# Kernel optimization log

Hardware: AMD Instinct MI355X
Metric: run time of the kernel (lower is better)

Reference implementation:

```python
import jax, jax.numpy as jnp
import numpy as np

B, S, IN, H, L = 512, 1024, 64, 32, 4


def setup_inputs() -> dict:
    key = jax.random.key(0)
    ks = jax.random.split(key, 9)
    s = 1.0 / np.sqrt(H)  # PyTorch RNN/Linear init scale
    u = lambda k, shape: jax.random.uniform(k, shape, jnp.float32, -s, s)
    return {
        "x": jax.random.normal(ks[0], (B, S, IN), jnp.float32),
        "h_state": jnp.zeros((L, B, H), jnp.float32),
        "W_ih0": u(ks[1], (H, IN)),          # layer 0 input weights
        "W_ih_rest": u(ks[2], (L - 1, H, H)),  # layers 1..3 input weights
        "W_hh": u(ks[3], (L, H, H)),
        "b_ih": u(ks[4], (L, H)),
        "b_hh": u(ks[5], (L, H)),
        "fc_w": u(ks[6], (1, H)),
        "fc_b": u(ks[7], (1,)),
    }


def _rnn_layer(seq_sbf, h0, W_ih, W_hh, b):
    # seq_sbf: [S, B, F]; vanilla RNN: h_t = tanh(x_t W_ih^T + h_{t-1} W_hh^T + b)
    def step(h, x_t):
        h = jnp.tanh(x_t @ W_ih.T + h @ W_hh.T + b)
        return h, h
    return jax.lax.scan(step, h0, seq_sbf)


def reference(x, h_state, W_ih0, W_ih_rest, W_hh, b_ih, b_hh, fc_w, fc_b):
    seq = jnp.swapaxes(x, 0, 1)  # [S, B, IN]
    h_finals = []
    for l in range(L):  # fixed small layer count
        W_ih = W_ih0 if l == 0 else W_ih_rest[l - 1]
        h_last, seq = _rnn_layer(seq, h_state[l], W_ih, W_hh[l], b_ih[l] + b_hh[l])
        h_finals.append(h_last)
    r_out = jnp.swapaxes(seq, 0, 1)                 # [B, S, H]
    logits = (r_out @ fc_w.T + fc_b)[..., 0]        # fused per-timestep Linear -> [B, S]
    probs = jax.nn.softmax(logits, axis=-1)         # nn.Softmax over last (seq) dim
    return probs, jnp.stack(h_finals, axis=0)       # [B,S], [L,B,H]
```

## Files before the change

kernel.cpp:

```cpp
#include <hip/hip_runtime.h>


#define BB 512
#define SS 1024
#define INF 64
#define HH 32
#define LL 4

typedef __fp16 v2h __attribute__((ext_vector_type(2)));

__device__ __forceinline__ v2h bch(unsigned u) { return __builtin_bit_cast(v2h, u); }
__device__ __forceinline__ unsigned bcu(v2h h) { return __builtin_bit_cast(unsigned, h); }

template <int CTRL>
__device__ __forceinline__ float dpp_add(float v) {
  int y = __builtin_amdgcn_update_dpp(0, __float_as_int(v), CTRL, 0xF, 0xF, true);
  return v + __int_as_float(y);
}
template <int CTRL>
__device__ __forceinline__ float dpp_mov(float v) {
  int y = __builtin_amdgcn_update_dpp(0, __float_as_int(v), CTRL, 0xF, 0xF, true);
  return __int_as_float(y);
}

__device__ __forceinline__ float tanh_fast(float a) {
  const float e = __builtin_amdgcn_exp2f(a * 2.885390081777927f);
  const float r = __builtin_amdgcn_rcpf(e + 1.0f);
  return __builtin_fmaf(-2.0f, r, 1.0f);
}

__device__ __forceinline__ float dot16p(const v2h* w, const v2h* v) {
  float a = 0.f, c = 0.f;
#pragma unroll
  for (int j = 0; j < 4; ++j) {
    a = __builtin_amdgcn_fdot2(w[2 * j + 0], v[2 * j + 0], a, false);
    c = __builtin_amdgcn_fdot2(w[2 * j + 1], v[2 * j + 1], c, false);
  }
  return a + c;
}

#define BAR() asm volatile("s_waitcnt lgkmcnt(0)\n\ts_barrier" ::: "memory")

__global__ __launch_bounds__(256) void u0_kernel(
    const float* __restrict__ x, const float* __restrict__ W_ih0,
    const float* __restrict__ b_ih, const float* __restrict__ b_hh,
    float* __restrict__ u0) {
  __shared__ float Wl[HH * INF];
  __shared__ float bl[HH];
  const int tid = threadIdx.x;
  {
    const float4* src = (const float4*)W_ih0;
    float4* dst = (float4*)Wl;
    dst[tid] = src[tid];
    dst[tid + 256] = src[tid + 256];
    if (tid < HH) bl[tid] = b_ih[tid] + b_hh[tid];
  }
  __syncthreads();

  const int row = blockIdx.x * 256 + tid;
  const float4* xr = (const float4*)(x + (size_t)row * INF);
  float acc[HH];
#pragma unroll
  for (int u = 0; u < HH; ++u) acc[u] = bl[u];
#pragma unroll 4
  for (int kc = 0; kc < 16; ++kc) {
    const float4 xv = xr[kc];
#pragma unroll
    for (int u = 0; u < HH; ++u) {
      const float4 wv = ((const float4*)Wl)[u * 16 + kc];
      acc[u] += wv.x * xv.x + wv.y * xv.y + wv.z * xv.z + wv.w * xv.w;
    }
  }
  float4* op = (float4*)(u0 + (size_t)row * HH);
#pragma unroll
  for (int j = 0; j < 8; ++j)
    op[j] = make_float4(acc[4 * j], acc[4 * j + 1], acc[4 * j + 2], acc[4 * j + 3]);
}

__global__ __launch_bounds__(256, 2) void rnn_kernel(
    const float* __restrict__ u0g_all, const float* __restrict__ h_state,
    const float* __restrict__ W_ih_rest, const float* __restrict__ W_hh,
    const float* __restrict__ b_ih, const float* __restrict__ b_hh,
    const float* __restrict__ fc_w, const float* __restrict__ fc_b,
    float* __restrict__ out) {
  __shared__ int hb[LL][2][8][16];
  __shared__ float h3f[2][8][32];
  __shared__ float lbuf[64];

  const int tid  = threadIdx.x;
  const int wid  = tid >> 6;
  const int lane = tid & 63;
  const int b    = blockIdx.x;
  const int ks   = lane & 1;
  const int h    = lane >> 1;

  v2h wih[8], whh[8];
  {
    const float2* ph = (const float2*)(W_hh + (size_t)(wid * HH + h) * HH + ks * 16);
#pragma unroll
    for (int j = 0; j < 8; ++j) whh[j] = __builtin_amdgcn_cvt_pkrtz(ph[j].x, ph[j].y);
  }
  float bias = 0.f;
  if (wid > 0) {
    const float2* pi =
        (const float2*)(W_ih_rest + (size_t)((wid - 1) * HH + h) * HH + ks * 16);
#pragma unroll
    for (int j = 0; j < 8; ++j) wih[j] = __builtin_amdgcn_cvt_pkrtz(pi[j].x, pi[j].y);
    bias = b_ih[wid * HH + h] + b_hh[wid * HH + h];
  }
  const float fcwh = fc_w[h] * 0.5f;
  const float fcb  = fc_b[0];

  v2h sv[8];
  {
    const float2* hs = (const float2*)(h_state + (size_t)(wid * BB + b) * HH);
#pragma unroll
    for (int j = 0; j < 8; ++j)
      sv[j] = __builtin_amdgcn_cvt_pkrtz(hs[ks * 8 + j].x, hs[ks * 8 + j].y);
  }

  const float* ug = u0g_all + (size_t)b * SS * HH;
  float* const outrow = out + (size_t)b * SS;
  float* const hfin   = out + (size_t)BB * SS;

  auto ld8 = [&](const int* p, v2h* v) __attribute__((always_inline)) {
    const uint4* q = (const uint4*)p;
    uint4 A = q[0], B = q[1];
    v[0] = bch(A.x); v[1] = bch(A.y); v[2] = bch(A.z); v[3] = bch(A.w);
    v[4] = bch(B.x); v[5] = bch(B.y); v[6] = bch(B.z); v[7] = bch(B.w);
  };
  auto packpair = [&](float hv) __attribute__((always_inline)) {
    return bcu(__builtin_amdgcn_cvt_pkrtz(hv, dpp_mov<0xEE>(hv)));
  };
  auto store_pk = [&](int l, int buf, int slot, unsigned pk) __attribute__((always_inline)) {
    if ((lane & 3) == 0) hb[l][buf][slot][lane >> 2] = (int)pk;
  };
  auto fcred = [&](float v) __attribute__((always_inline)) {
    v = dpp_add<0x111>(v);
    v = dpp_add<0x112>(v);
    v = dpp_add<0x114>(v);
    v = dpp_add<0x118>(v);
    v = dpp_add<0x142>(v);
    v = dpp_add<0x143>(v);
    return v;
  };

  if (wid == 0) {
    float urA[8], urB[8];
#pragma unroll
    for (int i = 0; i < 8; ++i) urA[i] = ug[i * HH + h];
    auto iter0 = [&](int n, int buf, float* urC, float* urN)
        __attribute__((always_inline)) {
      BAR();
      const bool fc_on = (n >= 4);
      const bool cw    = (n <= 127);
      float a[8];
      if (fc_on) {
#pragma unroll
        for (int i = 0; i < 8; ++i) a[i] = h3f[buf ^ 1][i][h];
      }
      if (cw) {
        const int tb = 8 * (n + 1);
#pragma unroll
        for (int i = 0; i < 8; ++i) {
          int t = tb + i; t = t < SS ? t : SS - 1;
          urN[i] = ug[t * HH + h];
        }
        float hv7 = 0.f;
#pragma unroll
        for (int i = 0; i < 8; ++i) {
          float acc = dot16p(whh, sv);
          acc = dpp_add<0xB1>(acc) + urC[i];
          const float hv = tanh_fast(acc);
          const unsigned pk = packpair(hv);
          store_pk(0, buf, i, pk);
          ld8(&hb[0][buf][i][ks * 8], sv);
          if (i == 7) hv7 = hv;
        }
        if (n == 127 && ks == 0) hfin[(0 * BB + b) * HH + h] = hv7;
      }
      if (fc_on) {
        const int tf0 = 8 * (n - 4);
#pragma unroll
        for (int i = 0; i < 8; ++i) {
          float v = fcred(a[i] * fcwh);
          if (lane == 63) lbuf[(tf0 + i) & 63] = v + fcb;
        }
        if (((n - 4) & 7) == 7) {
          float lv = lbuf[lane];
          outrow[(tf0 + 7) - 63 + lane] = lv;
        }
      }
    };
    for (int n0 = 0; n0 < 132; n0 += 2) {
      iter0(n0, 0, urA, urB);
      iter0(n0 + 1, 1, urB, urA);
    }
  } else {
    v2h vi[8][8];
    auto iterl = [&](int n, int buf) __attribute__((always_inline)) {
      BAR();
      const bool cw = (n >= wid && n <= 127 + wid);
      if (cw) {
#pragma unroll
        for (int i = 0; i < 8; ++i)
          ld8(&hb[wid - 1][buf ^ 1][i][ks * 8], vi[i]);
        float hv7 = 0.f;
#pragma unroll
        for (int i = 0; i < 8; ++i) {
          float acc = dot16p(wih, vi[i]) + dot16p(whh, sv);
          acc = dpp_add<0xB1>(acc) + bias;
          const float hv = tanh_fast(acc);
          const unsigned pk = packpair(hv);
          store_pk(wid, buf, i, pk);
          if (wid == 3 && ks == 0) h3f[buf][i][h] = hv;
          ld8(&hb[wid][buf][i][ks * 8], sv);
          if (i == 7) hv7 = hv;
        }
        if (n == 127 + wid && ks == 0) hfin[(wid * BB + b) * HH + h] = hv7;
      }
    };
    for (int n0 = 0; n0 < 132; n0 += 2) {
      iterl(n0, 0);
      iterl(n0 + 1, 1);
    }
  }
}

__global__ __launch_bounds__(256) void softmax_kernel(float* __restrict__ out) {
  __shared__ float red[8];
  const int row = blockIdx.x;
  float* p = out + (size_t)row * SS;
  const int tid = threadIdx.x;
  float4 v = ((const float4*)p)[tid];
  float m = fmaxf(fmaxf(v.x, v.y), fmaxf(v.z, v.w));
#pragma unroll
  for (int d = 32; d >= 1; d >>= 1) m = fmaxf(m, __shfl_xor(m, d));
  if ((tid & 63) == 0) red[tid >> 6] = m;
  __syncthreads();
  m = fmaxf(fmaxf(red[0], red[1]), fmaxf(red[2], red[3]));
  const float e0 = __expf(v.x - m), e1 = __expf(v.y - m);
  const float e2 = __expf(v.z - m), e3 = __expf(v.w - m);
  float s = (e0 + e1) + (e2 + e3);
#pragma unroll
  for (int d = 32; d >= 1; d >>= 1) s += __shfl_xor(s, d);
  if ((tid & 63) == 0) red[4 + (tid >> 6)] = s;
  __syncthreads();
  s = (red[4] + red[5]) + (red[6] + red[7]);
  const float inv = 1.0f / s;
  float4 o;
  o.x = e0 * inv; o.y = e1 * inv; o.z = e2 * inv; o.w = e3 * inv;
  ((float4*)p)[tid] = o;
}

extern "C" void kernel_launch(void* const* d_in, const int* in_sizes, int n_in,
                              void* d_out, int out_size, void* d_ws, size_t ws_size,
                              hipStream_t stream) {
  const float* x         = (const float*)d_in[0];
  const float* h_state   = (const float*)d_in[1];
  const float* W_ih0     = (const float*)d_in[2];
  const float* W_ih_rest = (const float*)d_in[3];
  const float* W_hh      = (const float*)d_in[4];
  const float* b_ih      = (const float*)d_in[5];
  const float* b_hh      = (const float*)d_in[6];
  const float* fc_w      = (const float*)d_in[7];
  const float* fc_b      = (const float*)d_in[8];
  float* out = (float*)d_out;
  float* u0  = (float*)d_ws;

  hipLaunchKernelGGL(u0_kernel, dim3((BB * SS) / 256), dim3(256), 0, stream,
                     x, W_ih0, b_ih, b_hh, u0);
  hipLaunchKernelGGL(rnn_kernel, dim3(BB), dim3(256), 0, stream,
                     u0, h_state, W_ih_rest, W_hh, b_ih, b_hh, fc_w, fc_b, out);
  hipLaunchKernelGGL(softmax_kernel, dim3(BB), dim3(256), 0, stream, out);
}
```

Baseline: 439.5 us.

## Double wavefront chunk size and fuse softmax into RNN kernel via shared logits

Raises the per-barrier timestep chunk from 8 to 16, which halves the number of block barriers in the layer-pipelined recurrence. Logits are now kept in a full shared-memory row instead of being flushed to global memory, and the softmax runs at the end of the RNN kernel, so the separate softmax launch and its global round trip go away. Layers 1-3 load the previous layer's inputs in groups of four with double buffering to limit register pressure. The trade-offs are a longer pipeline fill/drain per chunk, higher register and LDS use that may hurt occupancy, and more serial work after each barrier.

```diff
diff --git a/kernel.cpp b/kernel.cpp
--- a/kernel.cpp
+++ b/kernel.cpp
@@ -6,6 +6,7 @@
 #define INF 64
 #define HH 32
 #define LL 4
+#define KB 16
 
 typedef __fp16 v2h __attribute__((ext_vector_type(2)));
 
@@ -83,9 +84,10 @@
     const float* __restrict__ b_ih, const float* __restrict__ b_hh,
     const float* __restrict__ fc_w, const float* __restrict__ fc_b,
     float* __restrict__ out) {
-  __shared__ int hb[LL][2][8][16];
-  __shared__ float h3f[2][8][32];
-  __shared__ float lbuf[64];
+  __shared__ int hb[LL][2][KB][16];
+  __shared__ float h3f[2][KB][32];
+  __shared__ float lrow[SS];
+  __shared__ float red[8];
 
   const int tid  = threadIdx.x;
   const int wid  = tid >> 6;
@@ -120,8 +122,7 @@
   }
 
   const float* ug = u0g_all + (size_t)b * SS * HH;
-  float* const outrow = out + (size_t)b * SS;
-  float* const hfin   = out + (size_t)BB * SS;
+  float* const hfin = out + (size_t)BB * SS;
 
   auto ld8 = [&](const int* p, v2h* v) __attribute__((always_inline)) {
     const uint4* q = (const uint4*)p;
@@ -146,111 +147,119 @@
   };
 
   if (wid == 0) {
-    float urA[8], urB[8];
-#pragma unroll
-    for (int i = 0; i < 8; ++i) urA[i] = ug[i * HH + h];
+    float urA[KB], urB[KB];
+#pragma unroll
+    for (int i = 0; i < KB; ++i) urA[i] = ug[i * HH + h];
     auto iter0 = [&](int n, int buf, float* urC, float* urN)
         __attribute__((always_inline)) {
       BAR();
       const bool fc_on = (n >= 4);
-      const bool cw    = (n <= 127);
-      float a[8];
+      const bool cw    = (n <= 63);
+      float a[KB];
       if (fc_on) {
 #pragma unroll
-        for (int i = 0; i < 8; ++i) a[i] = h3f[buf ^ 1][i][h];
+        for (int i = 0; i < KB; ++i) a[i] = h3f[buf ^ 1][i][h];
       }
       if (cw) {
-        const int tb = 8 * (n + 1);
-#pragma unroll
-        for (int i = 0; i < 8; ++i) {
+        const int tb = KB * (n + 1);
+#pragma unroll
+        for (int i = 0; i < KB; ++i) {
           int t = tb + i; t = t < SS ? t : SS - 1;
           urN[i] = ug[t * HH + h];
         }
-        float hv7 = 0.f;
-#pragma unroll
-        for (int i = 0; i < 8; ++i) {
+        float hvL = 0.f;
+#pragma unroll
+        for (int i = 0; i < KB; ++i) {
           float acc = dot16p(whh, sv);
           acc = dpp_add<0xB1>(acc) + urC[i];
           const float hv = tanh_fast(acc);
           const unsigned pk = packpair(hv);
           store_pk(0, buf, i, pk);
           ld8(&hb[0][buf][i][ks * 8], sv);
-          if (i == 7) hv7 = hv;
+          if (i == KB - 1) hvL = hv;
         }
-        if (n == 127 && ks == 0) hfin[(0 * BB + b) * HH + h] = hv7;
+        if (n == 63 && ks == 0) hfin[(0 * BB + b) * HH + h] = hvL;
       }
       if (fc_on) {
-        const int tf0 = 8 * (n - 4);
-#pragma unroll
-        for (int i = 0; i < 8; ++i) {
+        const int tf0 = KB * (n - 4);
+#pragma unroll
+        for (int i = 0; i < KB; ++i) {
           float v = fcred(a[i] * fcwh);
-          if (lane == 63) lbuf[(tf0 + i) & 63] = v + fcb;
+          if (lane == 63) lrow[tf0 + i] = v + fcb;
         }
-        if (((n - 4) & 7) == 7) {
-          float lv = lbuf[lane];
-          outrow[(tf0 + 7) - 63 + lane] = lv;
-        }
-      }
-    };
-    for (int n0 = 0; n0 < 132; n0 += 2) {
+      }
+    };
+    for (int n0 = 0; n0 < 68; n0 += 2) {
       iter0(n0, 0, urA, urB);
       iter0(n0 + 1, 1, urB, urA);
     }
   } else {
-    v2h vi[8][8];
+    v2h viA[4][8], viB[4][8];
+    auto ldgrp = [&](int buf, int g, v2h (*vv)[8]) __attribute__((always_inline)) {
+#pragma unroll
+      for (int q = 0; q < 4; ++q)
+        ld8(&hb[wid - 1][buf ^ 1][g * 4 + q][ks * 8], vv[q]);
+    };
+    auto dogrp = [&](int n, int buf, int g, v2h (*vc)[8], float& hvL)
+        __attribute__((always_inline)) {
+#pragma unroll
+      for (int q = 0; q < 4; ++q) {
+        const int i = g * 4 + q;
+        float accA = dot16p(wih, vc[q]);
+        float acc = accA + dot16p(whh, sv);
+        acc = dpp_add<0xB1>(acc) + bias;
+        const float hv = tanh_fast(acc);
+        const unsigned pk = packpair(hv);
+        store_pk(wid, buf, i, pk);
+        if (wid == 3 && ks == 0) h3f[buf][i][h] = hv;
+        ld8(&hb[wid][buf][i][ks * 8], sv);
+        if (i == KB - 1) hvL = hv;
+      }
+    };
     auto iterl = [&](int n, int buf) __attribute__((always_inline)) {
       BAR();
-      const bool cw = (n >= wid && n <= 127 + wid);
+      const bool cw = (n >= wid && n <= 63 + wid);
       if (cw) {
-#pragma unroll
-        for (int i = 0; i < 8; ++i)
-          ld8(&hb[wid - 1][buf ^ 1][i][ks * 8], vi[i]);
-        float hv7 = 0.f;
-#pragma unroll
-        for (int i = 0; i < 8; ++i) {
-          float acc = dot16p(wih, vi[i]) + dot16p(whh, sv);
-          acc = dpp_add<0xB1>(acc) + bias;
-          const float hv = tanh_fast(acc);
-          const unsigned pk = packpair(hv);
-          store_pk(wid, buf, i, pk);
-          if (wid == 3 && ks == 0) h3f[buf][i][h] = hv;
-          ld8(&hb[wid][buf][i][ks * 8], sv);
-          if (i == 7) hv7 = hv;
-        }
-        if (n == 127 + wid && ks == 0) hfin[(wid * BB + b) * HH + h] = hv7;
-      }
-    };
-    for (int n0 = 0; n0 < 132; n0 += 2) {
+        float hvL = 0.f;
+        ldgrp(buf, 0, viA);
+        ldgrp(buf, 1, viB);
+        dogrp(n, buf, 0, viA, hvL);
+        ldgrp(buf, 2, viA);
+        dogrp(n, buf, 1, viB, hvL);
+        ldgrp(buf, 3, viB);
+        dogrp(n, buf, 2, viA, hvL);
+        dogrp(n, buf, 3, viB, hvL);
+        if (n == 63 + wid && ks == 0) hfin[(wid * BB + b) * HH + h] = hvL;
+      }
+    };
+    for (int n0 = 0; n0 < 68; n0 += 2) {
       iterl(n0, 0);
       iterl(n0 + 1, 1);
     }
   }
-}
-
-__global__ __launch_bounds__(256) void softmax_kernel(float* __restrict__ out) {
-  __shared__ float red[8];
-  const int row = blockIdx.x;
-  float* p = out + (size_t)row * SS;
-  const int tid = threadIdx.x;
-  float4 v = ((const float4*)p)[tid];
-  float m = fmaxf(fmaxf(v.x, v.y), fmaxf(v.z, v.w));
-#pragma unroll
-  for (int d = 32; d >= 1; d >>= 1) m = fmaxf(m, __shfl_xor(m, d));
-  if ((tid & 63) == 0) red[tid >> 6] = m;
+
   __syncthreads();
-  m = fmaxf(fmaxf(red[0], red[1]), fmaxf(red[2], red[3]));
-  const float e0 = __expf(v.x - m), e1 = __expf(v.y - m);
-  const float e2 = __expf(v.z - m), e3 = __expf(v.w - m);
-  float s = (e0 + e1) + (e2 + e3);
-#pragma unroll
-  for (int d = 32; d >= 1; d >>= 1) s += __shfl_xor(s, d);
-  if ((tid & 63) == 0) red[4 + (tid >> 6)] = s;
-  __syncthreads();
-  s = (red[4] + red[5]) + (red[6] + red[7]);
-  const float inv = 1.0f / s;
-  float4 o;
-  o.x = e0 * inv; o.y = e1 * inv; o.z = e2 * inv; o.w = e3 * inv;
-  ((float4*)p)[tid] = o;
+  {
+    float4 v = ((const float4*)lrow)[tid];
+    float m = fmaxf(fmaxf(v.x, v.y), fmaxf(v.z, v.w));
+#pragma unroll
+    for (int d = 32; d >= 1; d >>= 1) m = fmaxf(m, __shfl_xor(m, d));
+    if ((tid & 63) == 0) red[tid >> 6] = m;
+    __syncthreads();
+    m = fmaxf(fmaxf(red[0], red[1]), fmaxf(red[2], red[3]));
+    const float e0 = __expf(v.x - m), e1 = __expf(v.y - m);
+    const float e2 = __expf(v.z - m), e3 = __expf(v.w - m);
+    float s = (e0 + e1) + (e2 + e3);
+#pragma unroll
+    for (int d = 32; d >= 1; d >>= 1) s += __shfl_xor(s, d);
+    if ((tid & 63) == 0) red[4 + (tid >> 6)] = s;
+    __syncthreads();
+    s = (red[4] + red[5]) + (red[6] + red[7]);
+    const float inv = 1.0f / s;
+    float4 o;
+    o.x = e0 * inv; o.y = e1 * inv; o.z = e2 * inv; o.w = e3 * inv;
+    ((float4*)(out + (size_t)b * SS))[tid] = o;
+  }
 }
 
 extern "C" void kernel_launch(void* const* d_in, const int* in_sizes, int n_in,
@@ -272,5 +281,4 @@
                      x, W_ih0, b_ih, b_hh, u0);
   hipLaunchKernelGGL(rnn_kernel, dim3(BB), dim3(256), 0, stream,
                      u0, h_state, W_ih_rest, W_hh, b_ih, b_hh, fc_w, fc_b, out);
-  hipLaunchKernelGGL(softmax_kernel, dim3(BB), dim3(256), 0, stream, out);
-}
+}
```

After: 427.5 us. -2.7%, faster.
